# Optimization experiments

Hardware: AMD Instinct MI355X
Metric: run time of the kernel (lower is better)

The kernel has to match this reference:

```python
import jax, jax.numpy as jnp
import numpy as np


def batch_pairwise_dist(x, y):
    # x: (B, Nx, 3), y: (B, Ny, 3) -> P: (B, Nx, Ny) squared euclidean dists
    xx = jnp.sum(x * x, axis=-1)                      # (B, Nx)
    yy = jnp.sum(y * y, axis=-1)                      # (B, Ny)
    zz = jnp.einsum('bnd,bmd->bnm', x, y)             # (B, Nx, Ny)
    return xx[:, :, None] + yy[:, None, :] - 2.0 * zz


def huber(x, c):
    return jnp.where(x < c, 0.5 * x * x, c * x - 0.5 * c * c)


def global_align_loss(preds, gts, c):
    # preds, gts: (B, N, 3) point sets; faithful to GlobalAlignLoss.forward
    P = batch_pairwise_dist(gts, preds)               # (B, Ngt, Npred)
    loss_1 = jnp.sum(huber(jnp.min(P, axis=1), c))
    loss_2 = jnp.sum(huber(jnp.min(P, axis=2), c))
    return loss_1 + loss_2


def setup_inputs() -> dict:
    key = jax.random.key(0)
    ks = jax.random.split(key, 8)
    B, KP, K, N = 4, 512, 32, 4096
    return {
        'src_keypoints': jax.random.normal(ks[0], (B, 3, KP), dtype=jnp.float32),
        'tgt_keypoints': jax.random.normal(ks[1], (B, 3, KP), dtype=jnp.float32),
        'rotation_ab': jax.random.normal(ks[2], (B, 3, 3), dtype=jnp.float32),
        'translation_ab': jax.random.normal(ks[3], (B, 3), dtype=jnp.float32),
        'src_keypoints_knn': jax.random.normal(ks[4], (B, 3, KP, K), dtype=jnp.float32),
        'tgt_keypoints_knn': jax.random.normal(ks[5], (B, 3, KP, K), dtype=jnp.float32),
        'k': K,
        'src_transformed': jax.random.normal(ks[6], (B, 3, N), dtype=jnp.float32),
        'tgt': jax.random.normal(ks[7], (B, 3, N), dtype=jnp.float32),
    }


def reference(src_keypoints, tgt_keypoints, rotation_ab, translation_ab,
              src_keypoints_knn, tgt_keypoints_knn, k, src_transformed, tgt):
    margin = 0.01  # loss_margin from init
    # Global alignment loss on full clouds (points last -> points first)
    gal = global_align_loss(jnp.transpose(src_transformed, (0, 2, 1)),
                            jnp.transpose(tgt, (0, 2, 1)), margin)
    # se3.transform: p' = R @ p + t, applied to keypoints (B, 3, KP)
    transformed_srckps = jnp.einsum('bij,bjn->bin', rotation_ab, src_keypoints) \
        + translation_ab[:, :, None]
    keypoints_loss = jnp.sum((transformed_srckps - tgt_keypoints) ** 2)
    knn_consensus_loss = jnp.sum((src_keypoints_knn - tgt_keypoints_knn) ** 2)
    neighborhood_consensus_loss = knn_consensus_loss / k + keypoints_loss
    return (neighborhood_consensus_loss, gal)
```

## Files before the change

kernel.cpp:

```cpp
#include <hip/hip_runtime.h>

#define NPTS 4096
#define NB   4
#define KP   512
#define HUBER_C 0.01f
#define QCHUNK 128
#define NQC (NPTS / QCHUNK)
#define GAL_BLOCKS (2 * NB * NQC)
#define NPK (NPTS / 2)
#define NOG 16
#define PKG (NPK / NOG)
#define QPT 8
#define LDA_STRIDE (PKG + 1)
#define PMIN_STRIDE (QCHUNK + 4)

typedef float v2f __attribute__((ext_vector_type(2)));



__device__ inline float huber_f(float x) {
    return (x < HUBER_C) ? 0.5f * x * x
                         : fmaf(HUBER_C, x, -0.5f * HUBER_C * HUBER_C);
}

__device__ inline v2f splat2(float s) { v2f r; r.x = s; r.y = s; return r; }


__global__ void init_kernel(float* __restrict__ out) {
    if (threadIdx.x < 2) out[threadIdx.x] = 0.0f;
}

__global__ __launch_bounds__(256) void main_kernel(
    const float* __restrict__ srcT, const float* __restrict__ tgtT,
    const float* __restrict__ skp, const float* __restrict__ tkp,
    const float* __restrict__ R, const float* __restrict__ T,
    const float* __restrict__ aknn, const float* __restrict__ bknn,
    const int* __restrict__ kptr, float* __restrict__ out,
    int knn_blocks, int knn_quads)
{
    __shared__ float4 lds_a[NOG * LDA_STRIDE];
    __shared__ float4 lds_b[NOG * LDA_STRIDE];
    __shared__ float pminl[NOG * PMIN_STRIDE];
    __shared__ float red[4];

    const int bid = blockIdx.x;
    const int tid = threadIdx.x;
    float contrib = 0.0f;
    float* target;

    if (bid < GAL_BLOCKS) {
        const int qc  = bid & (NQC - 1);
        const int b   = (bid >> 5) & 3;
        const int dir = bid >> 7;
        const float* qb = (dir ? tgtT : srcT) + b * 3 * NPTS;
        const float* ob = (dir ? srcT : tgtT) + b * 3 * NPTS;

        #pragma unroll
        for (int k = 0; k < NPK / 256; ++k) {
            int idx = tid + k * 256;
            int j = 2 * idx;
            float2 X = *(const float2*)(ob + j);
            float2 Y = *(const float2*)(ob + NPTS + j);
            float2 Z = *(const float2*)(ob + 2 * NPTS + j);
            float w0 = fmaf(X.x, X.x, fmaf(Y.x, Y.x, Z.x * Z.x));
            float w1 = fmaf(X.y, X.y, fmaf(Y.y, Y.y, Z.y * Z.y));
            int li = idx + (idx >> 7);
            lds_a[li] = make_float4(X.x, X.y, Y.x, Y.y);
            lds_b[li] = make_float4(Z.x, Z.y, w0, w1);
        }

        const int ql0 = tid & 15;
        const int og  = tid >> 4;
        float ax[QPT], ay[QPT], az[QPT], qw[QPT];
        v2f mm[QPT];
        #pragma unroll
        for (int j = 0; j < QPT; ++j) {
            int q = qc * QCHUNK + ql0 + 16 * j;
            float x = qb[q], y = qb[NPTS + q], z = qb[2 * NPTS + q];
            ax[j] = -2.0f * x; ay[j] = -2.0f * y; az[j] = -2.0f * z;
            qw[j] = fmaf(x, x, fmaf(y, y, z * z));
            mm[j].x = 3.0e38f; mm[j].y = 3.0e38f;
        }
        __syncthreads();

        const float4* la = lds_a + og * LDA_STRIDE;
        const float4* lb = lds_b + og * LDA_STRIDE;
        #pragma unroll 4
        for (int p = 0; p < PKG; ++p) {
            float4 A = la[p], B = lb[p];
            v2f X, Y, Z, W;
            X.x = A.x; X.y = A.y; Y.x = A.z; Y.y = A.w;
            Z.x = B.x; Z.y = B.y; W.x = B.z; W.y = B.w;
            #pragma unroll
            for (int j = 0; j < QPT; ++j) {
                v2f t = __builtin_elementwise_fma(X, splat2(ax[j]),
                        __builtin_elementwise_fma(Y, splat2(ay[j]),
                        __builtin_elementwise_fma(Z, splat2(az[j]), W)));
                mm[j] = __builtin_elementwise_min(mm[j], t);
            }
        }

        #pragma unroll
        for (int j = 0; j < QPT; ++j)
            pminl[og * PMIN_STRIDE + ql0 + 16 * j] =
                fminf(mm[j].x, mm[j].y) + qw[j];
        __syncthreads();

        if (tid < QCHUNK) {
            float m = 3.0e38f;
            #pragma unroll
            for (int g = 0; g < NOG; ++g)
                m = fminf(m, pminl[g * PMIN_STRIDE + tid]);
            contrib = huber_f(m);
        }
        target = out + 1;
    } else if (bid < GAL_BLOCKS + knn_blocks) {
        int i = (bid - GAL_BLOCKS) * 256 + tid;
        if (i < knn_quads) {
            float4 va = ((const float4*)aknn)[i];
            float4 vb = ((const float4*)bknn)[i];
            float dx = va.x - vb.x, dy = va.y - vb.y;
            float dz = va.z - vb.z, dw = va.w - vb.w;
            contrib = fmaf(dx, dx, fmaf(dy, dy, fmaf(dz, dz, dw * dw)));
        }
        contrib *= 1.0f / (float)(*kptr);
        target = out;
    } else {
        int i = (bid - GAL_BLOCKS - knn_blocks) * 256 + tid;
        int b = i >> 9;
        int n = i & (KP - 1);
        const float* r = R + b * 9;
        const float* t = T + b * 3;
        const float* s = skp + b * 3 * KP;
        const float* g = tkp + b * 3 * KP;
        float sx = s[n], sy = s[KP + n], sz = s[2 * KP + n];
        #pragma unroll
        for (int d = 0; d < 3; ++d) {
            float v = fmaf(r[d*3+0], sx, fmaf(r[d*3+1], sy, fmaf(r[d*3+2], sz, t[d])))
                      - g[d * KP + n];
            contrib = fmaf(v, v, contrib);
        }
        target = out;
    }

    float v = contrib;
    #pragma unroll
    for (int off = 32; off; off >>= 1) v += __shfl_down(v, off, 64);
    if ((tid & 63) == 0) red[tid >> 6] = v;
    __syncthreads();
    if (tid == 0)
        atomicAdd(target, red[0] + red[1] + red[2] + red[3]);
}


extern "C" void kernel_launch(void* const* d_in, const int* in_sizes, int n_in,
                              void* d_out, int out_size, void* d_ws, size_t ws_size,
                              hipStream_t stream) {
    const float* skp  = (const float*)d_in[0];
    const float* tkp  = (const float*)d_in[1];
    const float* R    = (const float*)d_in[2];
    const float* T    = (const float*)d_in[3];
    const float* aknn = (const float*)d_in[4];
    const float* bknn = (const float*)d_in[5];
    const int*   kptr = (const int*)d_in[6];
    const float* srcT = (const float*)d_in[7];
    const float* tgtT = (const float*)d_in[8];
    float* out = (float*)d_out;

    const int knn_quads  = in_sizes[4] / 4;
    const int knn_blocks = (knn_quads + 255) / 256;
    const int kp_blocks  = (NB * KP + 255) / 256;
    const int total      = GAL_BLOCKS + knn_blocks + kp_blocks;

    init_kernel<<<1, 64, 0, stream>>>(out);
    main_kernel<<<total, 256, 0, stream>>>(
        srcT, tgtT, skp, tkp, R, T, aknn, bknn, kptr, out,
        knn_blocks, knn_quads);
}
```

Before: 86.29 us.

## Use 512-thread blocks with 16 queries per thread and shuffle min-reduction

Doubles the block size to 512 threads and reorganizes the chamfer work split: 8 query lanes by 64 point groups, each thread handling 16 queries over fewer points. Query coordinates are staged once in LDS instead of loaded by each thread from global memory. The per-group minima are combined with cross-lane shuffles before a small LDS reduction. The inner loop processes two points per iteration with scalar fminf. This raises per-thread register pressure and halves the number of blocks for the KNN and keypoint sections, which risks lower occupancy.

```diff
diff --git a/kernel.cpp b/kernel.cpp
--- a/kernel.cpp
+++ b/kernel.cpp
@@ -4,15 +4,16 @@
 #define NB   4
 #define KP   512
 #define HUBER_C 0.01f
+#define BT     512
 #define QCHUNK 128
 #define NQC (NPTS / QCHUNK)
 #define GAL_BLOCKS (2 * NB * NQC)
 #define NPK (NPTS / 2)
-#define NOG 16
+#define QL  8
+#define NOG (BT / QL)
 #define PKG (NPK / NOG)
-#define QPT 8
+#define QPT (QCHUNK / QL)
 #define LDA_STRIDE (PKG + 1)
-#define PMIN_STRIDE (QCHUNK + 4)
 
 typedef float v2f __attribute__((ext_vector_type(2)));
 
@@ -30,7 +31,7 @@
     if (threadIdx.x < 2) out[threadIdx.x] = 0.0f;
 }
 
-__global__ __launch_bounds__(256) void main_kernel(
+__global__ __launch_bounds__(BT, 2) void main_kernel(
     const float* __restrict__ srcT, const float* __restrict__ tgtT,
     const float* __restrict__ skp, const float* __restrict__ tkp,
     const float* __restrict__ R, const float* __restrict__ T,
@@ -40,8 +41,9 @@
 {
     __shared__ float4 lds_a[NOG * LDA_STRIDE];
     __shared__ float4 lds_b[NOG * LDA_STRIDE];
-    __shared__ float pminl[NOG * PMIN_STRIDE];
-    __shared__ float red[4];
+    __shared__ float4 qlds4[QCHUNK];
+    __shared__ float pm[BT / 64][QCHUNK + 4];
+    __shared__ float red[BT / 64];
 
     const int bid = blockIdx.x;
     const int tid = threadIdx.x;
@@ -56,66 +58,82 @@
         const float* ob = (dir ? srcT : tgtT) + b * 3 * NPTS;
 
         #pragma unroll
-        for (int k = 0; k < NPK / 256; ++k) {
-            int idx = tid + k * 256;
+        for (int k = 0; k < NPK / BT; ++k) {
+            int idx = tid + k * BT;
             int j = 2 * idx;
             float2 X = *(const float2*)(ob + j);
             float2 Y = *(const float2*)(ob + NPTS + j);
             float2 Z = *(const float2*)(ob + 2 * NPTS + j);
             float w0 = fmaf(X.x, X.x, fmaf(Y.x, Y.x, Z.x * Z.x));
             float w1 = fmaf(X.y, X.y, fmaf(Y.y, Y.y, Z.y * Z.y));
-            int li = idx + (idx >> 7);
+            int li = idx + (idx >> 5);
             lds_a[li] = make_float4(X.x, X.y, Y.x, Y.y);
             lds_b[li] = make_float4(Z.x, Z.y, w0, w1);
         }
-
-        const int ql0 = tid & 15;
-        const int og  = tid >> 4;
+        if (tid < QCHUNK) {
+            int q = qc * QCHUNK + tid;
+            float x = qb[q], y = qb[NPTS + q], z = qb[2 * NPTS + q];
+            qlds4[tid] = make_float4(-2.0f * x, -2.0f * y, -2.0f * z,
+                                     fmaf(x, x, fmaf(y, y, z * z)));
+        }
+        __syncthreads();
+
+        const int ql0 = tid & (QL - 1);
+        const int og  = tid >> 3;
         float ax[QPT], ay[QPT], az[QPT], qw[QPT];
         v2f mm[QPT];
         #pragma unroll
-        for (int j = 0; j < QPT; ++j) {
-            int q = qc * QCHUNK + ql0 + 16 * j;
-            float x = qb[q], y = qb[NPTS + q], z = qb[2 * NPTS + q];
-            ax[j] = -2.0f * x; ay[j] = -2.0f * y; az[j] = -2.0f * z;
-            qw[j] = fmaf(x, x, fmaf(y, y, z * z));
-            mm[j].x = 3.0e38f; mm[j].y = 3.0e38f;
-        }
-        __syncthreads();
+        for (int j2 = 0; j2 < QPT; ++j2) {
+            float4 Q = qlds4[ql0 + QL * j2];
+            ax[j2] = Q.x; ay[j2] = Q.y; az[j2] = Q.z; qw[j2] = Q.w;
+            mm[j2].x = 3.0e38f; mm[j2].y = 3.0e38f;
+        }
 
         const float4* la = lds_a + og * LDA_STRIDE;
         const float4* lb = lds_b + og * LDA_STRIDE;
-        #pragma unroll 4
-        for (int p = 0; p < PKG; ++p) {
-            float4 A = la[p], B = lb[p];
+        auto dist2 = [&](const float4& A, const float4& B, int j2) -> v2f {
             v2f X, Y, Z, W;
             X.x = A.x; X.y = A.y; Y.x = A.z; Y.y = A.w;
             Z.x = B.x; Z.y = B.y; W.x = B.z; W.y = B.w;
+            return __builtin_elementwise_fma(X, splat2(ax[j2]),
+                   __builtin_elementwise_fma(Y, splat2(ay[j2]),
+                   __builtin_elementwise_fma(Z, splat2(az[j2]), W)));
+        };
+        #pragma unroll 2
+        for (int p = 0; p < PKG; p += 2) {
+            float4 A0 = la[p], B0 = lb[p];
+            float4 A1 = la[p + 1], B1 = lb[p + 1];
             #pragma unroll
-            for (int j = 0; j < QPT; ++j) {
-                v2f t = __builtin_elementwise_fma(X, splat2(ax[j]),
-                        __builtin_elementwise_fma(Y, splat2(ay[j]),
-                        __builtin_elementwise_fma(Z, splat2(az[j]), W)));
-                mm[j] = __builtin_elementwise_min(mm[j], t);
+            for (int j2 = 0; j2 < QPT; ++j2) {
+                v2f t0 = dist2(A0, B0, j2);
+                v2f t1 = dist2(A1, B1, j2);
+                mm[j2].x = fminf(fminf(mm[j2].x, t0.x), t1.x);
+                mm[j2].y = fminf(fminf(mm[j2].y, t0.y), t1.y);
             }
         }
 
-        #pragma unroll
-        for (int j = 0; j < QPT; ++j)
-            pminl[og * PMIN_STRIDE + ql0 + 16 * j] =
-                fminf(mm[j].x, mm[j].y) + qw[j];
+        const int lane = tid & 63;
+        const int w = tid >> 6;
+        #pragma unroll
+        for (int j2 = 0; j2 < QPT; ++j2) {
+            float v = fminf(mm[j2].x, mm[j2].y);
+            v = fminf(v, __shfl_xor(v, 8, 64));
+            v = fminf(v, __shfl_xor(v, 16, 64));
+            v = fminf(v, __shfl_xor(v, 32, 64));
+            if (lane < QL) pm[w][ql0 + QL * j2] = v + qw[j2];
+        }
         __syncthreads();
 
         if (tid < QCHUNK) {
             float m = 3.0e38f;
             #pragma unroll
-            for (int g = 0; g < NOG; ++g)
-                m = fminf(m, pminl[g * PMIN_STRIDE + tid]);
+            for (int w2 = 0; w2 < BT / 64; ++w2)
+                m = fminf(m, pm[w2][tid]);
             contrib = huber_f(m);
         }
         target = out + 1;
     } else if (bid < GAL_BLOCKS + knn_blocks) {
-        int i = (bid - GAL_BLOCKS) * 256 + tid;
+        int i = (bid - GAL_BLOCKS) * BT + tid;
         if (i < knn_quads) {
             float4 va = ((const float4*)aknn)[i];
             float4 vb = ((const float4*)bknn)[i];
@@ -126,7 +144,7 @@
         contrib *= 1.0f / (float)(*kptr);
         target = out;
     } else {
-        int i = (bid - GAL_BLOCKS - knn_blocks) * 256 + tid;
+        int i = (bid - GAL_BLOCKS - knn_blocks) * BT + tid;
         int b = i >> 9;
         int n = i & (KP - 1);
         const float* r = R + b * 9;
@@ -148,8 +166,12 @@
     for (int off = 32; off; off >>= 1) v += __shfl_down(v, off, 64);
     if ((tid & 63) == 0) red[tid >> 6] = v;
     __syncthreads();
-    if (tid == 0)
-        atomicAdd(target, red[0] + red[1] + red[2] + red[3]);
+    if (tid == 0) {
+        float s = 0.0f;
+        #pragma unroll
+        for (int w2 = 0; w2 < BT / 64; ++w2) s += red[w2];
+        atomicAdd(target, s);
+    }
 }
 
 
@@ -168,12 +190,12 @@
     float* out = (float*)d_out;
 
     const int knn_quads  = in_sizes[4] / 4;
-    const int knn_blocks = (knn_quads + 255) / 256;
-    const int kp_blocks  = (NB * KP + 255) / 256;
+    const int knn_blocks = (knn_quads + BT - 1) / BT;
+    const int kp_blocks  = (NB * KP + BT - 1) / BT;
     const int total      = GAL_BLOCKS + knn_blocks + kp_blocks;
 
     init_kernel<<<1, 64, 0, stream>>>(out);
-    main_kernel<<<total, 256, 0, stream>>>(
+    main_kernel<<<total, BT, 0, stream>>>(
         srcT, tgtT, skp, tkp, R, T, aknn, bknn, kptr, out,
         knn_blocks, knn_quads);
 }
```

Measured after the change: 86.57 us. No clear change (+0.3%).
